# Kernel tuning notes

Measured on AMD Instinct MI355X. Metric: run time of the kernel, lower is better.

The kernel has to match this reference:

```python
import jax, jax.numpy as jnp
import numpy as np

N = 131072
IN, HID, OUT = 128, 256, 64
NUM_TASKS = 16
NUM_COPIES = 4
NUM_LAYERS = 3


def setup_inputs() -> dict:
    key = jax.random.key(0)
    ks = jax.random.split(key, 10)
    inputs = jax.random.normal(ks[0], (N, IN), dtype=jnp.float32)
    task_indices = jax.random.randint(ks[1], (N,), 0, NUM_TASKS, dtype=jnp.int32)
    copy_maps = jax.random.randint(ks[2], (NUM_LAYERS, NUM_TASKS), 0, NUM_COPIES, dtype=jnp.int32)
    # per-copy Linear weights, Kaiming-ish scale 1/sqrt(fan_in)
    W0 = jax.random.normal(ks[3], (NUM_COPIES, IN, HID), dtype=jnp.float32) / np.sqrt(IN)
    b0 = jax.random.normal(ks[4], (NUM_COPIES, HID), dtype=jnp.float32) * 0.01
    W1 = jax.random.normal(ks[5], (NUM_COPIES, HID, HID), dtype=jnp.float32) / np.sqrt(HID)
    b1 = jax.random.normal(ks[6], (NUM_COPIES, HID), dtype=jnp.float32) * 0.01
    W2 = jax.random.normal(ks[7], (NUM_COPIES, HID, OUT), dtype=jnp.float32) / np.sqrt(HID)
    b2 = jax.random.normal(ks[8], (NUM_COPIES, OUT), dtype=jnp.float32) * 0.01
    return {"inputs": inputs, "task_indices": task_indices, "copy_maps": copy_maps,
            "W0": W0, "b0": b0, "W1": W1, "b1": b1, "W2": W2, "b2": b2}


def _routed_layer(x, W, b, copy_idx, apply_tanh):
    # x: [N, d_in], W: [C, d_in, d_out], b: [C, d_out], copy_idx: [N]
    # Each token goes through exactly one copy's Linear. Equivalent to the
    # torch sort->per-copy-forward->unsort, expressed as masked accumulation
    # over the small fixed set of copies (avoids data-dependent shapes).
    y = jnp.zeros((x.shape[0], W.shape[2]), dtype=x.dtype)
    for c in range(W.shape[0]):
        mask = (copy_idx == c).astype(x.dtype)[:, None]  # [N, 1]
        y = y + mask * (x @ W[c] + b[c])
    return jnp.tanh(y) if apply_tanh else y


def reference(inputs, task_indices, copy_maps, W0, b0, W1, b1, W2, b2):
    x = inputs
    Ws = (W0, W1, W2)
    bs = (b0, b1, b2)
    for layer in range(NUM_LAYERS):
        copy_idx = copy_maps[layer][task_indices]  # [N] task->copy routing
        x = _routed_layer(x, Ws[layer], bs[layer], copy_idx,
                          apply_tanh=(layer != NUM_LAYERS - 1))
    return x
```

## Files before the change

kernel.cpp:

```cpp
#include <hip/hip_runtime.h>

#define N_TOK 131072
#define TILE 64
#define NT_MAX 2064
#define XS 136
#define HS 264

typedef __attribute__((ext_vector_type(8))) short s8v;
typedef __attribute__((ext_vector_type(4))) short s4v;
typedef __attribute__((ext_vector_type(4))) float f4v;
typedef unsigned short ushort_t;

__device__ __forceinline__ unsigned short f2bf(float x) {
    union { float f; unsigned u; } v; v.f = x;
    unsigned r = v.u + 0x7fffu + ((v.u >> 16) & 1u);
    return (unsigned short)(r >> 16);
}

__device__ __forceinline__ float tanh_fast(float x) {
    float e = __expf(2.0f * x);
    return 1.0f - 2.0f / (e + 1.0f);
}

__global__ void prep_hist_kernel(const float* __restrict__ W0, const float* __restrict__ W1,
                                 const float* __restrict__ W2,
                                 ushort_t* __restrict__ W0p, ushort_t* __restrict__ W1p,
                                 ushort_t* __restrict__ W2p,
                                 const int* __restrict__ task, int* __restrict__ blockCounts) {
    if (blockIdx.x < 224) {
        int f = blockIdx.x * 256 + threadIdx.x;
        const float* src; ushort_t* dst; int K, N;
        if (f < 16384)      { src = W0; dst = W0p; K = 128; N = 256; }
        else if (f < 49152) { src = W1; dst = W1p; K = 256; N = 256; f -= 16384; }
        else                { src = W2; dst = W2p; K = 256; N = 64;  f -= 49152; }
        int fpc = (N >> 4) * (K >> 5) * 64;
        int c = f / fpc, r = f % fpc;
        int lane = r & 63;
        int kt = (r >> 6) % (K >> 5);
        int ftile = (r >> 6) / (K >> 5);
        int n = ftile * 16 + (lane & 15);
        int kbase = kt * 32 + (lane >> 4) * 8;
        const float* s = src + (size_t)c * K * N + (size_t)kbase * N + n;
        s8v pk;
#pragma unroll
        for (int j = 0; j < 8; j++) pk[j] = (short)f2bf(s[(size_t)j * N]);
        *reinterpret_cast<s8v*>(dst + ((size_t)(c * fpc + r) << 3)) = pk;
    } else {
        __shared__ int cnt[16];
        int t = threadIdx.x;
        int hb = blockIdx.x - 224;
        if (t < 16) cnt[t] = 0;
        __syncthreads();
        int base = hb * 2048 + t;
#pragma unroll
        for (int i = 0; i < 8; i++) atomicAdd(&cnt[task[base + i * 256]], 1);
        __syncthreads();
        if (t < 16) blockCounts[hb * 16 + t] = cnt[t];
    }
}

__global__ void sort_kernel(const int* __restrict__ task, const int* __restrict__ blockCounts,
                            int* __restrict__ tileTask, int* __restrict__ nT,
                            int* __restrict__ perm) {
    __shared__ int cntLds[1024];
    __shared__ int total[16], pref[16], rank[16];
    __shared__ int tokBase[16], tbase[17];
    int t = threadIdx.x, b = blockIdx.x;
    for (int i = t; i < 1024; i += 256) cntLds[i] = blockCounts[i];
    if (t < 16) rank[t] = 0;
    __syncthreads();
    if (t < 16) {
        int tot = 0, pf = 0;
#pragma unroll
        for (int bb = 0; bb < 64; bb++) {
            int v = cntLds[bb * 16 + t];
            tot += v;
            if (bb < b) pf += v;
        }
        total[t] = tot; pref[t] = pf;
    }
    __syncthreads();
    if (t == 0) {
        int tok = 0, tile = 0;
        for (int k = 0; k < 16; k++) {
            tokBase[k] = tok;
            tbase[k] = tile;
            int ntk = (total[k] + TILE - 1) / TILE;
            tok += ntk * TILE;
            tile += ntk;
        }
        tbase[16] = tile;
        if (b == 0) nT[0] = tile;
    }
    __syncthreads();
    if (b == 0) {
        for (int i = t; i < NT_MAX; i += 256) {
            int tk = 0;
            if (i < tbase[16]) {
#pragma unroll
                for (int k = 0; k < 16; k++) if (i >= tbase[k]) tk = k;
            }
            tileTask[i] = tk;
        }
    }
    int tk[8], my[8];
#pragma unroll
    for (int i = 0; i < 8; i++) {
        int idx = b * 2048 + i * 256 + t;
        tk[i] = task[idx];
        my[i] = atomicAdd(&rank[tk[i]], 1);
    }
#pragma unroll
    for (int i = 0; i < 8; i++) {
        int idx = b * 2048 + i * 256 + t;
        perm[tokBase[tk[i]] + pref[tk[i]] + my[i]] = idx;
    }
}

__launch_bounds__(512, 4)
__global__ void mlp_kernel(const float* __restrict__ x_in,
                           const int* __restrict__ cmap,
                           const float* __restrict__ b0,
                           const float* __restrict__ b1,
                           const float* __restrict__ b2,
                           const ushort_t* __restrict__ W0p,
                           const ushort_t* __restrict__ W1p,
                           const ushort_t* __restrict__ W2p,
                           const int* __restrict__ tileTask,
                           const int* __restrict__ nTp,
                           const int* __restrict__ perm,
                           float* __restrict__ out) {
    __shared__ __align__(16) ushort_t bufA[TILE * HS];
    __shared__ __align__(16) ushort_t bufB[TILE * HS];
    __shared__ int toks[TILE];

    int b = blockIdx.x;
    if (b >= nTp[0]) return;
    int t = threadIdx.x;
    int task = tileTask[b];
    int c0 = cmap[task], c1 = cmap[16 + task], c2 = cmap[32 + task];

    {
        int r = t >> 3, q = t & 7;
        int tok = perm[b * TILE + r];
        if (q == 0) toks[r] = tok;
        float4 v[4];
        if ((unsigned)tok < (unsigned)N_TOK) {
            const float4* src = reinterpret_cast<const float4*>(x_in) + (size_t)tok * 32 + q * 4;
#pragma unroll
            for (int i = 0; i < 4; i++) v[i] = src[i];
        } else {
#pragma unroll
            for (int i = 0; i < 4; i++) v[i] = make_float4(0.f, 0.f, 0.f, 0.f);
        }
        ushort_t* dst = &bufA[r * XS + q * 16];
#pragma unroll
        for (int i = 0; i < 2; i++) {
            float4 va = v[2 * i], vb = v[2 * i + 1];
            s8v pk;
            pk[0] = (short)f2bf(va.x); pk[1] = (short)f2bf(va.y);
            pk[2] = (short)f2bf(va.z); pk[3] = (short)f2bf(va.w);
            pk[4] = (short)f2bf(vb.x); pk[5] = (short)f2bf(vb.y);
            pk[6] = (short)f2bf(vb.z); pk[7] = (short)f2bf(vb.w);
            *reinterpret_cast<s8v*>(dst + i * 8) = pk;
        }
    }
    __syncthreads();

    int w = t >> 6;
    int lane = t & 63;
    int l15 = lane & 15, lq = lane >> 4;

    {
        f4v acc[2][4];
#pragma unroll
        for (int mi = 0; mi < 2; mi++)
#pragma unroll
            for (int nt = 0; nt < 4; nt++) { f4v z = {0.f, 0.f, 0.f, 0.f}; acc[mi][nt] = z; }
        const ushort_t* Wc = W0p + (size_t)c0 * 32768;
#pragma unroll
        for (int kt = 0; kt < 4; kt++) {
            s8v xb[4];
#pragma unroll
            for (int nt = 0; nt < 4; nt++)
                xb[nt] = *reinterpret_cast<const s8v*>(&bufA[(nt * 16 + l15) * XS + kt * 32 + lq * 8]);
            s8v wa[2];
#pragma unroll
            for (int mi = 0; mi < 2; mi++)
                wa[mi] = *reinterpret_cast<const s8v*>(Wc + ((((2 * w + mi) * 4 + kt) * 64 + lane) << 3));
#pragma unroll
            for (int mi = 0; mi < 2; mi++)
#pragma unroll
                for (int nt = 0; nt < 4; nt++)
                    acc[mi][nt] = __builtin_amdgcn_mfma_f32_16x16x32_bf16(wa[mi], xb[nt], acc[mi][nt], 0, 0, 0);
        }
#pragma unroll
        for (int mi = 0; mi < 2; mi++) {
            int fbase = (2 * w + mi) * 16 + lq * 4;
            float4 bv = *reinterpret_cast<const float4*>(b0 + c0 * 256 + fbase);
            float br[4] = {bv.x, bv.y, bv.z, bv.w};
#pragma unroll
            for (int nt = 0; nt < 4; nt++) {
                s4v pk;
#pragma unroll
                for (int rg = 0; rg < 4; rg++)
                    pk[rg] = (short)f2bf(tanh_fast(acc[mi][nt][rg] + br[rg]));
                *reinterpret_cast<s4v*>(&bufB[(nt * 16 + l15) * HS + fbase]) = pk;
            }
        }
    }
    __syncthreads();

    {
        f4v acc[2][4];
#pragma unroll
        for (int mi = 0; mi < 2; mi++)
#pragma unroll
            for (int nt = 0; nt < 4; nt++) { f4v z = {0.f, 0.f, 0.f, 0.f}; acc[mi][nt] = z; }
        const ushort_t* Wc = W1p + (size_t)c1 * 65536;
#pragma unroll
        for (int kt = 0; kt < 8; kt++) {
            s8v xb[4];
#pragma unroll
            for (int nt = 0; nt < 4; nt++)
                xb[nt] = *reinterpret_cast<const s8v*>(&bufB[(nt * 16 + l15) * HS + kt * 32 + lq * 8]);
            s8v wa[2];
#pragma unroll
            for (int mi = 0; mi < 2; mi++)
                wa[mi] = *reinterpret_cast<const s8v*>(Wc + ((((2 * w + mi) * 8 + kt) * 64 + lane) << 3));
#pragma unroll
            for (int mi = 0; mi < 2; mi++)
#pragma unroll
                for (int nt = 0; nt < 4; nt++)
                    acc[mi][nt] = __builtin_amdgcn_mfma_f32_16x16x32_bf16(wa[mi], xb[nt], acc[mi][nt], 0, 0, 0);
        }
#pragma unroll
        for (int mi = 0; mi < 2; mi++) {
            int fbase = (2 * w + mi) * 16 + lq * 4;
            float4 bv = *reinterpret_cast<const float4*>(b1 + c1 * 256 + fbase);
            float br[4] = {bv.x, bv.y, bv.z, bv.w};
#pragma unroll
            for (int nt = 0; nt < 4; nt++) {
                s4v pk;
#pragma unroll
                for (int rg = 0; rg < 4; rg++)
                    pk[rg] = (short)f2bf(tanh_fast(acc[mi][nt][rg] + br[rg]));
                *reinterpret_cast<s4v*>(&bufA[(nt * 16 + l15) * HS + fbase]) = pk;
            }
        }
    }
    __syncthreads();

    {
        int mti = w & 3, half = w >> 2;
        f4v acc2[2];
#pragma unroll
        for (int j = 0; j < 2; j++) { f4v z = {0.f, 0.f, 0.f, 0.f}; acc2[j] = z; }
        const ushort_t* Wc = W2p + (size_t)c2 * 16384;
#pragma unroll
        for (int kt = 0; kt < 8; kt++) {
            s8v xb[2];
#pragma unroll
            for (int j = 0; j < 2; j++) {
                int nt = half * 2 + j;
                xb[j] = *reinterpret_cast<const s8v*>(&bufA[(nt * 16 + l15) * HS + kt * 32 + lq * 8]);
            }
            s8v wa = *reinterpret_cast<const s8v*>(Wc + (((mti * 8 + kt) * 64 + lane) << 3));
#pragma unroll
            for (int j = 0; j < 2; j++)
                acc2[j] = __builtin_amdgcn_mfma_f32_16x16x32_bf16(wa, xb[j], acc2[j], 0, 0, 0);
        }
        int fbase = mti * 16 + lq * 4;
        float4 bv = *reinterpret_cast<const float4*>(b2 + c2 * 64 + fbase);
#pragma unroll
        for (int j = 0; j < 2; j++) {
            int row = (half * 2 + j) * 16 + l15;
            int tok = toks[row];
            if ((unsigned)tok < (unsigned)N_TOK) {
                float4 o;
                o.x = acc2[j][0] + bv.x; o.y = acc2[j][1] + bv.y;
                o.z = acc2[j][2] + bv.z; o.w = acc2[j][3] + bv.w;
                *reinterpret_cast<float4*>(out + (size_t)tok * 64 + fbase) = o;
            }
        }
    }
}

extern "C" void kernel_launch(void* const* d_in, const int* in_sizes, int n_in,
                              void* d_out, int out_size, void* d_ws, size_t ws_size,
                              hipStream_t stream) {
    const float* inputs = (const float*)d_in[0];
    const int*   task   = (const int*)d_in[1];
    const int*   cmap   = (const int*)d_in[2];
    const float* W0     = (const float*)d_in[3];
    const float* b0     = (const float*)d_in[4];
    const float* W1     = (const float*)d_in[5];
    const float* b1     = (const float*)d_in[6];
    const float* W2     = (const float*)d_in[7];
    const float* b2     = (const float*)d_in[8];
    float* out = (float*)d_out;

    char* ws = (char*)d_ws;
    int* blockCounts = (int*)(ws + 0);
    int* nT          = (int*)(ws + 4096);
    int* tileTask    = (int*)(ws + 4160);
    int* perm        = (int*)(ws + 12416);
    ushort_t* W0p    = (ushort_t*)(ws + 540800);
    ushort_t* W1p    = (ushort_t*)(ws + 802944);
    ushort_t* W2p    = (ushort_t*)(ws + 1327232);

    prep_hist_kernel<<<288, 256, 0, stream>>>(W0, W1, W2, W0p, W1p, W2p, task, blockCounts);
    sort_kernel<<<64, 256, 0, stream>>>(task, blockCounts, tileTask, nT, perm);
    mlp_kernel<<<NT_MAX, 512, 0, stream>>>(inputs, cmap, b0, b1, b2,
                                           W0p, W1p, W2p, tileTask, nT, perm, out);
}
```

Measured before the change: 179.3 us.

## Give each wave its own 16 tokens across all features, tile of 128

Repartitions the MLP so each wave owns 16 tokens and computes all output features for them, keeping hidden activations in a per-wave LDS slot. Tokens are read straight from global memory into MFMA operands, which drops the shared input staging buffer. The tile grows to 128 tokens and occupancy drops to 2 blocks. In exchange, every wave streams the full weight matrices from cache, multiplying weight traffic per token. Register pressure also rises, with 16 accumulators per wave.

After: 267.8 us. 49.4% more time.

```diff
diff --git a/kernel.cpp b/kernel.cpp
--- a/kernel.cpp
+++ b/kernel.cpp
@@ -1,10 +1,10 @@
 #include <hip/hip_runtime.h>
 
 #define N_TOK 131072
-#define TILE 64
-#define NT_MAX 2064
-#define XS 136
+#define TILE 128
+#define NT_MAX 1040
 #define HS 264
+#define SLOT 8448
 
 typedef __attribute__((ext_vector_type(8))) short s8v;
 typedef __attribute__((ext_vector_type(4))) short s4v;
@@ -117,7 +117,7 @@
     }
 }
 
-__launch_bounds__(512, 4)
+__launch_bounds__(512, 2)
 __global__ void mlp_kernel(const float* __restrict__ x_in,
                            const int* __restrict__ cmap,
                            const float* __restrict__ b0,
@@ -130,9 +130,7 @@
                            const int* __restrict__ nTp,
                            const int* __restrict__ perm,
                            float* __restrict__ out) {
-    __shared__ __align__(16) ushort_t bufA[TILE * HS];
-    __shared__ __align__(16) ushort_t bufB[TILE * HS];
-    __shared__ int toks[TILE];
+    __shared__ __align__(16) ushort_t lds[8 * SLOT];
 
     int b = blockIdx.x;
     if (b >= nTp[0]) return;
@@ -140,147 +138,101 @@
     int task = tileTask[b];
     int c0 = cmap[task], c1 = cmap[16 + task], c2 = cmap[32 + task];
 
-    {
-        int r = t >> 3, q = t & 7;
-        int tok = perm[b * TILE + r];
-        if (q == 0) toks[r] = tok;
-        float4 v[4];
-        if ((unsigned)tok < (unsigned)N_TOK) {
-            const float4* src = reinterpret_cast<const float4*>(x_in) + (size_t)tok * 32 + q * 4;
-#pragma unroll
-            for (int i = 0; i < 4; i++) v[i] = src[i];
-        } else {
-#pragma unroll
-            for (int i = 0; i < 4; i++) v[i] = make_float4(0.f, 0.f, 0.f, 0.f);
-        }
-        ushort_t* dst = &bufA[r * XS + q * 16];
-#pragma unroll
-        for (int i = 0; i < 2; i++) {
-            float4 va = v[2 * i], vb = v[2 * i + 1];
-            s8v pk;
-            pk[0] = (short)f2bf(va.x); pk[1] = (short)f2bf(va.y);
-            pk[2] = (short)f2bf(va.z); pk[3] = (short)f2bf(va.w);
-            pk[4] = (short)f2bf(vb.x); pk[5] = (short)f2bf(vb.y);
-            pk[6] = (short)f2bf(vb.z); pk[7] = (short)f2bf(vb.w);
-            *reinterpret_cast<s8v*>(dst + i * 8) = pk;
-        }
-    }
-    __syncthreads();
-
     int w = t >> 6;
     int lane = t & 63;
     int l15 = lane & 15, lq = lane >> 4;
 
+    ushort_t* H1 = &lds[w * SLOT];
+    ushort_t* H2 = H1 + 4224;
+
+    int tok = perm[b * TILE + w * 16 + l15];
+    bool valid = (unsigned)tok < (unsigned)N_TOK;
+
     {
-        f4v acc[2][4];
-#pragma unroll
-        for (int mi = 0; mi < 2; mi++)
-#pragma unroll
-            for (int nt = 0; nt < 4; nt++) { f4v z = {0.f, 0.f, 0.f, 0.f}; acc[mi][nt] = z; }
+        f4v acc[16];
+#pragma unroll
+        for (int mt = 0; mt < 16; mt++) { f4v z = {0.f, 0.f, 0.f, 0.f}; acc[mt] = z; }
         const ushort_t* Wc = W0p + (size_t)c0 * 32768;
 #pragma unroll
         for (int kt = 0; kt < 4; kt++) {
-            s8v xb[4];
-#pragma unroll
-            for (int nt = 0; nt < 4; nt++)
-                xb[nt] = *reinterpret_cast<const s8v*>(&bufA[(nt * 16 + l15) * XS + kt * 32 + lq * 8]);
-            s8v wa[2];
-#pragma unroll
-            for (int mi = 0; mi < 2; mi++)
-                wa[mi] = *reinterpret_cast<const s8v*>(Wc + ((((2 * w + mi) * 4 + kt) * 64 + lane) << 3));
-#pragma unroll
-            for (int mi = 0; mi < 2; mi++)
-#pragma unroll
-                for (int nt = 0; nt < 4; nt++)
-                    acc[mi][nt] = __builtin_amdgcn_mfma_f32_16x16x32_bf16(wa[mi], xb[nt], acc[mi][nt], 0, 0, 0);
-        }
-#pragma unroll
-        for (int mi = 0; mi < 2; mi++) {
-            int fbase = (2 * w + mi) * 16 + lq * 4;
-            float4 bv = *reinterpret_cast<const float4*>(b0 + c0 * 256 + fbase);
-            float br[4] = {bv.x, bv.y, bv.z, bv.w};
-#pragma unroll
-            for (int nt = 0; nt < 4; nt++) {
-                s4v pk;
-#pragma unroll
-                for (int rg = 0; rg < 4; rg++)
-                    pk[rg] = (short)f2bf(tanh_fast(acc[mi][nt][rg] + br[rg]));
-                *reinterpret_cast<s4v*>(&bufB[(nt * 16 + l15) * HS + fbase]) = pk;
-            }
+            float4 u0 = make_float4(0.f, 0.f, 0.f, 0.f), u1 = u0;
+            if (valid) {
+                const float4* src = reinterpret_cast<const float4*>(x_in + (size_t)tok * 128 + kt * 32 + lq * 8);
+                u0 = src[0]; u1 = src[1];
+            }
+            s8v xb;
+            xb[0] = (short)f2bf(u0.x); xb[1] = (short)f2bf(u0.y);
+            xb[2] = (short)f2bf(u0.z); xb[3] = (short)f2bf(u0.w);
+            xb[4] = (short)f2bf(u1.x); xb[5] = (short)f2bf(u1.y);
+            xb[6] = (short)f2bf(u1.z); xb[7] = (short)f2bf(u1.w);
+#pragma unroll
+            for (int mt = 0; mt < 16; mt++) {
+                s8v wa = *reinterpret_cast<const s8v*>(Wc + (((mt * 4 + kt) * 64 + lane) << 3));
+                acc[mt] = __builtin_amdgcn_mfma_f32_16x16x32_bf16(wa, xb, acc[mt], 0, 0, 0);
+            }
+        }
+#pragma unroll
+        for (int mt = 0; mt < 16; mt++) {
+            float4 bv = *reinterpret_cast<const float4*>(b0 + c0 * 256 + mt * 16 + lq * 4);
+            s4v pk;
+            pk[0] = (short)f2bf(tanh_fast(acc[mt][0] + bv.x));
+            pk[1] = (short)f2bf(tanh_fast(acc[mt][1] + bv.y));
+            pk[2] = (short)f2bf(tanh_fast(acc[mt][2] + bv.z));
+            pk[3] = (short)f2bf(tanh_fast(acc[mt][3] + bv.w));
+            *reinterpret_cast<s4v*>(&H1[l15 * HS + mt * 16 + lq * 4]) = pk;
         }
     }
     __syncthreads();
 
     {
-        f4v acc[2][4];
-#pragma unroll
-        for (int mi = 0; mi < 2; mi++)
-#pragma unroll
-            for (int nt = 0; nt < 4; nt++) { f4v z = {0.f, 0.f, 0.f, 0.f}; acc[mi][nt] = z; }
+        f4v acc[16];
+#pragma unroll
+        for (int mt = 0; mt < 16; mt++) { f4v z = {0.f, 0.f, 0.f, 0.f}; acc[mt] = z; }
         const ushort_t* Wc = W1p + (size_t)c1 * 65536;
 #pragma unroll
         for (int kt = 0; kt < 8; kt++) {
-            s8v xb[4];
-#pragma unroll
-            for (int nt = 0; nt < 4; nt++)
-                xb[nt] = *reinterpret_cast<const s8v*>(&bufB[(nt * 16 + l15) * HS + kt * 32 + lq * 8]);
-            s8v wa[2];
-#pragma unroll
-            for (int mi = 0; mi < 2; mi++)
-                wa[mi] = *reinterpret_cast<const s8v*>(Wc + ((((2 * w + mi) * 8 + kt) * 64 + lane) << 3));
-#pragma unroll
-            for (int mi = 0; mi < 2; mi++)
-#pragma unroll
-                for (int nt = 0; nt < 4; nt++)
-                    acc[mi][nt] = __builtin_amdgcn_mfma_f32_16x16x32_bf16(wa[mi], xb[nt], acc[mi][nt], 0, 0, 0);
-        }
-#pragma unroll
-        for (int mi = 0; mi < 2; mi++) {
-            int fbase = (2 * w + mi) * 16 + lq * 4;
-            float4 bv = *reinterpret_cast<const float4*>(b1 + c1 * 256 + fbase);
-            float br[4] = {bv.x, bv.y, bv.z, bv.w};
-#pragma unroll
-            for (int nt = 0; nt < 4; nt++) {
-                s4v pk;
-#pragma unroll
-                for (int rg = 0; rg < 4; rg++)
-                    pk[rg] = (short)f2bf(tanh_fast(acc[mi][nt][rg] + br[rg]));
-                *reinterpret_cast<s4v*>(&bufA[(nt * 16 + l15) * HS + fbase]) = pk;
-            }
+            s8v xb = *reinterpret_cast<const s8v*>(&H1[l15 * HS + kt * 32 + lq * 8]);
+#pragma unroll
+            for (int mt = 0; mt < 16; mt++) {
+                s8v wa = *reinterpret_cast<const s8v*>(Wc + (((mt * 8 + kt) * 64 + lane) << 3));
+                acc[mt] = __builtin_amdgcn_mfma_f32_16x16x32_bf16(wa, xb, acc[mt], 0, 0, 0);
+            }
+        }
+#pragma unroll
+        for (int mt = 0; mt < 16; mt++) {
+            float4 bv = *reinterpret_cast<const float4*>(b1 + c1 * 256 + mt * 16 + lq * 4);
+            s4v pk;
+            pk[0] = (short)f2bf(tanh_fast(acc[mt][0] + bv.x));
+            pk[1] = (short)f2bf(tanh_fast(acc[mt][1] + bv.y));
+            pk[2] = (short)f2bf(tanh_fast(acc[mt][2] + bv.z));
+            pk[3] = (short)f2bf(tanh_fast(acc[mt][3] + bv.w));
+            *reinterpret_cast<s4v*>(&H2[l15 * HS + mt * 16 + lq * 4]) = pk;
         }
     }
     __syncthreads();
 
     {
-        int mti = w & 3, half = w >> 2;
-        f4v acc2[2];
-#pragma unroll
-        for (int j = 0; j < 2; j++) { f4v z = {0.f, 0.f, 0.f, 0.f}; acc2[j] = z; }
+        f4v acc[4];
+#pragma unroll
+        for (int mt = 0; mt < 4; mt++) { f4v z = {0.f, 0.f, 0.f, 0.f}; acc[mt] = z; }
         const ushort_t* Wc = W2p + (size_t)c2 * 16384;
 #pragma unroll
         for (int kt = 0; kt < 8; kt++) {
-            s8v xb[2];
-#pragma unroll
-            for (int j = 0; j < 2; j++) {
-                int nt = half * 2 + j;
-                xb[j] = *reinterpret_cast<const s8v*>(&bufA[(nt * 16 + l15) * HS + kt * 32 + lq * 8]);
-            }
-            s8v wa = *reinterpret_cast<const s8v*>(Wc + (((mti * 8 + kt) * 64 + lane) << 3));
-#pragma unroll
-            for (int j = 0; j < 2; j++)
-                acc2[j] = __builtin_amdgcn_mfma_f32_16x16x32_bf16(wa, xb[j], acc2[j], 0, 0, 0);
-        }
-        int fbase = mti * 16 + lq * 4;
-        float4 bv = *reinterpret_cast<const float4*>(b2 + c2 * 64 + fbase);
-#pragma unroll
-        for (int j = 0; j < 2; j++) {
-            int row = (half * 2 + j) * 16 + l15;
-            int tok = toks[row];
-            if ((unsigned)tok < (unsigned)N_TOK) {
+            s8v xb = *reinterpret_cast<const s8v*>(&H2[l15 * HS + kt * 32 + lq * 8]);
+#pragma unroll
+            for (int mt = 0; mt < 4; mt++) {
+                s8v wa = *reinterpret_cast<const s8v*>(Wc + (((mt * 8 + kt) * 64 + lane) << 3));
+                acc[mt] = __builtin_amdgcn_mfma_f32_16x16x32_bf16(wa, xb, acc[mt], 0, 0, 0);
+            }
+        }
+        if (valid) {
+#pragma unroll
+            for (int mt = 0; mt < 4; mt++) {
+                float4 bv = *reinterpret_cast<const float4*>(b2 + c2 * 64 + mt * 16 + lq * 4);
                 float4 o;
-                o.x = acc2[j][0] + bv.x; o.y = acc2[j][1] + bv.y;
-                o.z = acc2[j][2] + bv.z; o.w = acc2[j][3] + bv.w;
-                *reinterpret_cast<float4*>(out + (size_t)tok * 64 + fbase) = o;
+                o.x = acc[mt][0] + bv.x; o.y = acc[mt][1] + bv.y;
+                o.z = acc[mt][2] + bv.z; o.w = acc[mt][3] + bv.w;
+                *reinterpret_cast<float4*>(out + (size_t)tok * 64 + mt * 16 + lq * 4) = o;
             }
         }
     }
@@ -304,7 +256,7 @@
     int* blockCounts = (int*)(ws + 0);
     int* nT          = (int*)(ws + 4096);
     int* tileTask    = (int*)(ws + 4160);
-    int* perm        = (int*)(ws + 12416);
+    int* perm        = (int*)(ws + 8320);
     ushort_t* W0p    = (ushort_t*)(ws + 540800);
     ushort_t* W1p    = (ushort_t*)(ws + 802944);
     ushort_t* W2p    = (ushort_t*)(ws + 1327232);
```

## Halve token tile to 32 and store activations in MFMA fragment order

Applied to the files above, without the earlier changes.

The token tile shrinks from 64 to 32 rows, and the launch-bounds occupancy hint rises from 4 to 8 blocks per CU. The padded row-major LDS buffers become fragment-ordered buffers, so each lane reads its B operand as one contiguous 16-byte vector. bf16 packing switches to a cheaper round-half-up two-value pack, and workspace offsets grow to hold the larger tile count. The goal is more resident blocks and less LDS padding and bank-conflict overhead. The cost is that twice as many tiles each re-read the full per-copy weight set from L2, which doubles weight traffic.

Result: faster. 175.3 us (-2.2%).

```diff
diff --git a/kernel.cpp b/kernel.cpp
--- a/kernel.cpp
+++ b/kernel.cpp
@@ -1,13 +1,10 @@
 #include <hip/hip_runtime.h>
 
 #define N_TOK 131072
-#define TILE 64
-#define NT_MAX 2064
-#define XS 136
-#define HS 264
+#define TILE 32
+#define NT_MAX 4112
 
 typedef __attribute__((ext_vector_type(8))) short s8v;
-typedef __attribute__((ext_vector_type(4))) short s4v;
 typedef __attribute__((ext_vector_type(4))) float f4v;
 typedef unsigned short ushort_t;
 
@@ -15,6 +12,11 @@
     union { float f; unsigned u; } v; v.f = x;
     unsigned r = v.u + 0x7fffu + ((v.u >> 16) & 1u);
     return (unsigned short)(r >> 16);
+}
+
+__device__ __forceinline__ unsigned pk2(float a, float b) {
+    union { float f; unsigned u; } x, y; x.f = a; y.f = b;
+    return ((x.u + 0x8000u) >> 16) | ((y.u + 0x8000u) & 0xffff0000u);
 }
 
 __device__ __forceinline__ float tanh_fast(float x) {
@@ -117,7 +119,7 @@
     }
 }
 
-__launch_bounds__(512, 4)
+__launch_bounds__(512, 8)
 __global__ void mlp_kernel(const float* __restrict__ x_in,
                            const int* __restrict__ cmap,
                            const float* __restrict__ b0,
@@ -130,8 +132,8 @@
                            const int* __restrict__ nTp,
                            const int* __restrict__ perm,
                            float* __restrict__ out) {
-    __shared__ __align__(16) ushort_t bufA[TILE * HS];
-    __shared__ __align__(16) ushort_t bufB[TILE * HS];
+    __shared__ __align__(16) ushort_t H1[8192];
+    __shared__ __align__(16) ushort_t XH2[8192];
     __shared__ int toks[TILE];
 
     int b = blockIdx.x;
@@ -140,148 +142,131 @@
     int task = tileTask[b];
     int c0 = cmap[task], c1 = cmap[16 + task], c2 = cmap[32 + task];
 
-    {
-        int r = t >> 3, q = t & 7;
-        int tok = perm[b * TILE + r];
-        if (q == 0) toks[r] = tok;
-        float4 v[4];
-        if ((unsigned)tok < (unsigned)N_TOK) {
-            const float4* src = reinterpret_cast<const float4*>(x_in) + (size_t)tok * 32 + q * 4;
-#pragma unroll
-            for (int i = 0; i < 4; i++) v[i] = src[i];
-        } else {
-#pragma unroll
-            for (int i = 0; i < 4; i++) v[i] = make_float4(0.f, 0.f, 0.f, 0.f);
-        }
-        ushort_t* dst = &bufA[r * XS + q * 16];
-#pragma unroll
-        for (int i = 0; i < 2; i++) {
-            float4 va = v[2 * i], vb = v[2 * i + 1];
-            s8v pk;
-            pk[0] = (short)f2bf(va.x); pk[1] = (short)f2bf(va.y);
-            pk[2] = (short)f2bf(va.z); pk[3] = (short)f2bf(va.w);
-            pk[4] = (short)f2bf(vb.x); pk[5] = (short)f2bf(vb.y);
-            pk[6] = (short)f2bf(vb.z); pk[7] = (short)f2bf(vb.w);
-            *reinterpret_cast<s8v*>(dst + i * 8) = pk;
-        }
-    }
-    __syncthreads();
-
     int w = t >> 6;
     int lane = t & 63;
     int l15 = lane & 15, lq = lane >> 4;
 
     {
-        f4v acc[2][4];
+        int r = t >> 4, q = t & 15;
+        int tok = perm[b * TILE + r];
+        if (q == 0) toks[r] = tok;
+        float4 v0 = make_float4(0.f, 0.f, 0.f, 0.f), v1 = v0;
+        if ((unsigned)tok < (unsigned)N_TOK) {
+            const float4* src = reinterpret_cast<const float4*>(x_in) + (size_t)tok * 32 + q * 2;
+            v0 = src[0]; v1 = src[1];
+        }
+        int fragid = (r >> 4) * 4 + (q >> 2);
+        int lanep = (r & 15) + 16 * (q & 3);
+        uint4 pk;
+        pk.x = pk2(v0.x, v0.y); pk.y = pk2(v0.z, v0.w);
+        pk.z = pk2(v1.x, v1.y); pk.w = pk2(v1.z, v1.w);
+        *reinterpret_cast<uint4*>(&XH2[(fragid * 64 + lanep) << 3]) = pk;
+    }
+    __syncthreads();
+
+    {
+        f4v acc[2][2];
 #pragma unroll
         for (int mi = 0; mi < 2; mi++)
 #pragma unroll
-            for (int nt = 0; nt < 4; nt++) { f4v z = {0.f, 0.f, 0.f, 0.f}; acc[mi][nt] = z; }
+            for (int nt = 0; nt < 2; nt++) { f4v z = {0.f, 0.f, 0.f, 0.f}; acc[mi][nt] = z; }
         const ushort_t* Wc = W0p + (size_t)c0 * 32768;
 #pragma unroll
         for (int kt = 0; kt < 4; kt++) {
-            s8v xb[4];
-#pragma unroll
-            for (int nt = 0; nt < 4; nt++)
-                xb[nt] = *reinterpret_cast<const s8v*>(&bufA[(nt * 16 + l15) * XS + kt * 32 + lq * 8]);
             s8v wa[2];
 #pragma unroll
             for (int mi = 0; mi < 2; mi++)
                 wa[mi] = *reinterpret_cast<const s8v*>(Wc + ((((2 * w + mi) * 4 + kt) * 64 + lane) << 3));
+            s8v xb[2];
+#pragma unroll
+            for (int nt = 0; nt < 2; nt++)
+                xb[nt] = *reinterpret_cast<const s8v*>(&XH2[((nt * 4 + kt) * 64 + lane) << 3]);
 #pragma unroll
             for (int mi = 0; mi < 2; mi++)
 #pragma unroll
-                for (int nt = 0; nt < 4; nt++)
+                for (int nt = 0; nt < 2; nt++)
                     acc[mi][nt] = __builtin_amdgcn_mfma_f32_16x16x32_bf16(wa[mi], xb[nt], acc[mi][nt], 0, 0, 0);
         }
 #pragma unroll
         for (int mi = 0; mi < 2; mi++) {
-            int fbase = (2 * w + mi) * 16 + lq * 4;
-            float4 bv = *reinterpret_cast<const float4*>(b0 + c0 * 256 + fbase);
-            float br[4] = {bv.x, bv.y, bv.z, bv.w};
-#pragma unroll
-            for (int nt = 0; nt < 4; nt++) {
-                s4v pk;
-#pragma unroll
-                for (int rg = 0; rg < 4; rg++)
-                    pk[rg] = (short)f2bf(tanh_fast(acc[mi][nt][rg] + br[rg]));
-                *reinterpret_cast<s4v*>(&bufB[(nt * 16 + l15) * HS + fbase]) = pk;
+            int ft = 2 * w + mi;
+            float4 bv = *reinterpret_cast<const float4*>(b0 + c0 * 256 + ft * 16 + lq * 4);
+            int kt_h = ft >> 1;
+            int lanep = l15 + 16 * ((ft & 1) * 2 + (lq >> 1));
+            int j0 = (lq & 1) * 4;
+#pragma unroll
+            for (int nt = 0; nt < 2; nt++) {
+                float t0 = tanh_fast(acc[mi][nt][0] + bv.x);
+                float t1 = tanh_fast(acc[mi][nt][1] + bv.y);
+                float t2 = tanh_fast(acc[mi][nt][2] + bv.z);
+                float t3 = tanh_fast(acc[mi][nt][3] + bv.w);
+                uint2 pk; pk.x = pk2(t0, t1); pk.y = pk2(t2, t3);
+                *reinterpret_cast<uint2*>(&H1[(((nt * 8 + kt_h) * 64 + lanep) << 3) + j0]) = pk;
             }
         }
     }
     __syncthreads();
 
     {
-        f4v acc[2][4];
+        f4v acc[2][2];
 #pragma unroll
         for (int mi = 0; mi < 2; mi++)
 #pragma unroll
-            for (int nt = 0; nt < 4; nt++) { f4v z = {0.f, 0.f, 0.f, 0.f}; acc[mi][nt] = z; }
+            for (int nt = 0; nt < 2; nt++) { f4v z = {0.f, 0.f, 0.f, 0.f}; acc[mi][nt] = z; }
         const ushort_t* Wc = W1p + (size_t)c1 * 65536;
 #pragma unroll
         for (int kt = 0; kt < 8; kt++) {
-            s8v xb[4];
-#pragma unroll
-            for (int nt = 0; nt < 4; nt++)
-                xb[nt] = *reinterpret_cast<const s8v*>(&bufB[(nt * 16 + l15) * HS + kt * 32 + lq * 8]);
             s8v wa[2];
 #pragma unroll
             for (int mi = 0; mi < 2; mi++)
                 wa[mi] = *reinterpret_cast<const s8v*>(Wc + ((((2 * w + mi) * 8 + kt) * 64 + lane) << 3));
+            s8v xb[2];
+#pragma unroll
+            for (int nt = 0; nt < 2; nt++)
+                xb[nt] = *reinterpret_cast<const s8v*>(&H1[((nt * 8 + kt) * 64 + lane) << 3]);
 #pragma unroll
             for (int mi = 0; mi < 2; mi++)
 #pragma unroll
-                for (int nt = 0; nt < 4; nt++)
+                for (int nt = 0; nt < 2; nt++)
                     acc[mi][nt] = __builtin_amdgcn_mfma_f32_16x16x32_bf16(wa[mi], xb[nt], acc[mi][nt], 0, 0, 0);
         }
 #pragma unroll
         for (int mi = 0; mi < 2; mi++) {
-            int fbase = (2 * w + mi) * 16 + lq * 4;
-            float4 bv = *reinterpret_cast<const float4*>(b1 + c1 * 256 + fbase);
-            float br[4] = {bv.x, bv.y, bv.z, bv.w};
-#pragma unroll
-            for (int nt = 0; nt < 4; nt++) {
-                s4v pk;
-#pragma unroll
-                for (int rg = 0; rg < 4; rg++)
-                    pk[rg] = (short)f2bf(tanh_fast(acc[mi][nt][rg] + br[rg]));
-                *reinterpret_cast<s4v*>(&bufA[(nt * 16 + l15) * HS + fbase]) = pk;
+            int ft = 2 * w + mi;
+            float4 bv = *reinterpret_cast<const float4*>(b1 + c1 * 256 + ft * 16 + lq * 4);
+            int kt_h = ft >> 1;
+            int lanep = l15 + 16 * ((ft & 1) * 2 + (lq >> 1));
+            int j0 = (lq & 1) * 4;
+#pragma unroll
+            for (int nt = 0; nt < 2; nt++) {
+                float t0 = tanh_fast(acc[mi][nt][0] + bv.x);
+                float t1 = tanh_fast(acc[mi][nt][1] + bv.y);
+                float t2 = tanh_fast(acc[mi][nt][2] + bv.z);
+                float t3 = tanh_fast(acc[mi][nt][3] + bv.w);
+                uint2 pk; pk.x = pk2(t0, t1); pk.y = pk2(t2, t3);
+                *reinterpret_cast<uint2*>(&XH2[(((nt * 8 + kt_h) * 64 + lanep) << 3) + j0]) = pk;
             }
         }
     }
     __syncthreads();
 
     {
-        int mti = w & 3, half = w >> 2;
-        f4v acc2[2];
-#pragma unroll
-        for (int j = 0; j < 2; j++) { f4v z = {0.f, 0.f, 0.f, 0.f}; acc2[j] = z; }
+        int mt = w & 3, nt = w >> 2;
+        f4v acc = {0.f, 0.f, 0.f, 0.f};
         const ushort_t* Wc = W2p + (size_t)c2 * 16384;
 #pragma unroll
         for (int kt = 0; kt < 8; kt++) {
-            s8v xb[2];
-#pragma unroll
-            for (int j = 0; j < 2; j++) {
-                int nt = half * 2 + j;
-                xb[j] = *reinterpret_cast<const s8v*>(&bufA[(nt * 16 + l15) * HS + kt * 32 + lq * 8]);
-            }
-            s8v wa = *reinterpret_cast<const s8v*>(Wc + (((mti * 8 + kt) * 64 + lane) << 3));
-#pragma unroll
-            for (int j = 0; j < 2; j++)
-                acc2[j] = __builtin_amdgcn_mfma_f32_16x16x32_bf16(wa, xb[j], acc2[j], 0, 0, 0);
-        }
-        int fbase = mti * 16 + lq * 4;
-        float4 bv = *reinterpret_cast<const float4*>(b2 + c2 * 64 + fbase);
-#pragma unroll
-        for (int j = 0; j < 2; j++) {
-            int row = (half * 2 + j) * 16 + l15;
-            int tok = toks[row];
-            if ((unsigned)tok < (unsigned)N_TOK) {
-                float4 o;
-                o.x = acc2[j][0] + bv.x; o.y = acc2[j][1] + bv.y;
-                o.z = acc2[j][2] + bv.z; o.w = acc2[j][3] + bv.w;
-                *reinterpret_cast<float4*>(out + (size_t)tok * 64 + fbase) = o;
-            }
+            s8v wa = *reinterpret_cast<const s8v*>(Wc + (((mt * 8 + kt) * 64 + lane) << 3));
+            s8v xb = *reinterpret_cast<const s8v*>(&XH2[((nt * 8 + kt) * 64 + lane) << 3]);
+            acc = __builtin_amdgcn_mfma_f32_16x16x32_bf16(wa, xb, acc, 0, 0, 0);
+        }
+        int tok = toks[nt * 16 + l15];
+        if ((unsigned)tok < (unsigned)N_TOK) {
+            float4 bv = *reinterpret_cast<const float4*>(b2 + c2 * 64 + mt * 16 + lq * 4);
+            float4 o;
+            o.x = acc[0] + bv.x; o.y = acc[1] + bv.y;
+            o.z = acc[2] + bv.z; o.w = acc[3] + bv.w;
+            *reinterpret_cast<float4*>(out + (size_t)tok * 64 + mt * 16 + lq * 4) = o;
         }
     }
 }
@@ -304,10 +289,10 @@
     int* blockCounts = (int*)(ws + 0);
     int* nT          = (int*)(ws + 4096);
     int* tileTask    = (int*)(ws + 4160);
-    int* perm        = (int*)(ws + 12416);
-    ushort_t* W0p    = (ushort_t*)(ws + 540800);
-    ushort_t* W1p    = (ushort_t*)(ws + 802944);
-    ushort_t* W2p    = (ushort_t*)(ws + 1327232);
+    int* perm        = (int*)(ws + 20608);
+    ushort_t* W0p    = (ushort_t*)(ws + 546944);
+    ushort_t* W1p    = (ushort_t*)(ws + 809088);
+    ushort_t* W2p    = (ushort_t*)(ws + 1333376);
 
     prep_hist_kernel<<<288, 256, 0, stream>>>(W0, W1, W2, W0p, W1p, W2p, task, blockCounts);
     sort_kernel<<<64, 256, 0, stream>>>(task, blockCounts, tileTask, nT, perm);
```
